# Kernel optimization log

Hardware: AMD Instinct MI355X
Metric: run time of the kernel (lower is better)

## Reference

```python
import jax, jax.numpy as jnp
import numpy as np

N_NODES = 100000
N_EDGES = 1200000
D_IN = 64
D_HID = 64
BN_EPS = 1e-5


def setup_inputs() -> dict:
    key = jax.random.key(0)
    ks = jax.random.split(key, 16)
    x = jax.random.normal(ks[0], (N_NODES, D_IN), dtype=jnp.float32)
    edge_index = jax.random.randint(ks[1], (2, N_EDGES), 0, N_NODES, dtype=jnp.int64)
    s = 1.0 / np.sqrt(D_HID)
    W1 = jax.random.uniform(ks[2], (D_IN, D_HID), jnp.float32, -s, s)
    b1 = jax.random.uniform(ks[3], (D_HID,), jnp.float32, -s, s)
    W2 = jax.random.uniform(ks[4], (D_HID, D_HID), jnp.float32, -s, s)
    b2 = jax.random.uniform(ks[5], (D_HID,), jnp.float32, -s, s)
    W3 = jax.random.uniform(ks[6], (D_HID, D_HID), jnp.float32, -s, s)
    b3 = jax.random.uniform(ks[7], (D_HID,), jnp.float32, -s, s)
    gamma1 = jnp.ones((D_HID,), jnp.float32)
    beta1 = jnp.zeros((D_HID,), jnp.float32)
    gamma2 = jnp.ones((D_HID,), jnp.float32)
    beta2 = jnp.zeros((D_HID,), jnp.float32)
    return {"x": x, "edge_index": edge_index, "batch_size": 1,
            "W1": W1, "b1": b1, "gamma1": gamma1, "beta1": beta1,
            "W2": W2, "b2": b2, "gamma2": gamma2, "beta2": beta2,
            "W3": W3, "b3": b3}


def _gcn_norm(edge_index, n):
    # PyG GCNConv: add self-loops, symmetric normalization D^-1/2 (A+I) D^-1/2
    loop = jnp.arange(n, dtype=edge_index.dtype)
    src = jnp.concatenate([edge_index[0], loop])
    dst = jnp.concatenate([edge_index[1], loop])
    deg = jax.ops.segment_sum(jnp.ones_like(dst, dtype=jnp.float32), dst, num_segments=n)
    dinv = jnp.where(deg > 0, jax.lax.rsqrt(jnp.maximum(deg, 1.0)), 0.0)
    norm = dinv[src] * dinv[dst]  # [E + N]
    return src, dst, norm


def _gcn_conv(h, W, b, src, dst, norm, n):
    h = h @ W                      # [N, D]
    msg = h[src] * norm[:, None]   # gather + scale, [E+N, D]
    out = jax.ops.segment_sum(msg, dst, num_segments=n)  # scatter-add
    return out + b


def _bn_train(h, gamma, beta):
    # BatchNorm1d over nodes, training-mode (biased batch statistics)
    m = h.mean(axis=0)
    v = h.var(axis=0)
    return (h - m) * jax.lax.rsqrt(v + BN_EPS) * gamma + beta


def reference(x, edge_index, batch_size,
              W1, b1, gamma1, beta1, W2, b2, gamma2, beta2, W3, b3):
    n = x.shape[0]
    src, dst, norm = _gcn_norm(edge_index, n)
    h = _gcn_conv(x, W1, b1, src, dst, norm, n)
    h = jax.nn.relu(_bn_train(h, gamma1, beta1))
    h = _gcn_conv(h, W2, b2, src, dst, norm, n)
    h = jax.nn.relu(_bn_train(h, gamma2, beta2))
    h = _gcn_conv(h, W3, b3, src, dst, norm, n)
    return h  # output_type == 'hidden'
```

## Files before the change

kernel.cpp:

```cpp
#include <hip/hip_runtime.h>
#include <hip/hip_bf16.h>

#define D 64

typedef __attribute__((ext_vector_type(8))) short bf16x8;
typedef __attribute__((ext_vector_type(8))) unsigned short u16x8;
typedef __attribute__((ext_vector_type(4))) float f32x4;

__device__ __forceinline__ short f2bf(float x) {
    unsigned u = __float_as_uint(x);
    unsigned r = (u + 0x7fffu + ((u >> 16) & 1u)) >> 16;
    return (short)r;
}
__device__ __forceinline__ float bf2f(unsigned short u) {
    return __uint_as_float((unsigned)u << 16);
}

__global__ void detect_kernel(const unsigned int* e32, int* flag) {
    __shared__ int nz;
    if (threadIdx.x == 0) nz = 0;
    __syncthreads();
    if (e32[2 * threadIdx.x + 1] != 0) nz = 1;
    __syncthreads();
    if (threadIdx.x == 0) *flag = (nz == 0) ? 1 : 0;
}

__device__ __forceinline__ int load_idx(const void* e, int is64, long long i) {
    if (is64) return (int)((const long long*)e)[i];
    return ((const int*)e)[i];
}

#define NBLK 256

__global__ __launch_bounds__(256) void bucket_count_kernel(
    const void* edges, const int* flag, int* pbh, int E, int shift) {
    __shared__ int h[512];
    for (int i = threadIdx.x; i < 512; i += 256) h[i] = 0;
    __syncthreads();
    int is64 = *flag;
    int chunk = (E + gridDim.x - 1) / gridDim.x;
    int s0 = blockIdx.x * chunk;
    int s1 = min(E, s0 + chunk);
    for (int e = s0 + (int)threadIdx.x; e < s1; e += 256) {
        int d = load_idx(edges, is64, (long long)E + e);
        atomicAdd(&h[d >> shift], 1);
    }
    __syncthreads();
    for (int i = threadIdx.x; i < 512; i += 256) pbh[blockIdx.x * 512 + i] = h[i];
}

__global__ __launch_bounds__(256) void colscan_kernel(int* pbh, int* btot) {
    int b = blockIdx.x;
    int k = threadIdx.x;
    __shared__ int sA[256], sB[256];
    int v = pbh[k * 512 + b];
    sA[k] = v;
    __syncthreads();
    int* src = sA;
    int* dst = sB;
    for (int d = 1; d < 256; d <<= 1) {
        dst[k] = src[k] + (k >= d ? src[k - d] : 0);
        __syncthreads();
        int* t = src; src = dst; dst = t;
    }
    pbh[k * 512 + b] = src[k] - v;
    if (k == 255) btot[b] = src[255];
}

__global__ __launch_bounds__(512) void basescan_kernel(const int* btot, int* bbase, int E) {
    __shared__ int sA[512], sB[512];
    int b = threadIdx.x;
    int v = btot[b];
    sA[b] = v;
    __syncthreads();
    int* src = sA;
    int* dst = sB;
    for (int d = 1; d < 512; d <<= 1) {
        dst[b] = src[b] + (b >= d ? src[b - d] : 0);
        __syncthreads();
        int* t = src; src = dst; dst = t;
    }
    bbase[b] = src[b] - v;
    if (b == 0) bbase[512] = E;
}

__global__ __launch_bounds__(256) void bucket_scatter_kernel(
    const void* edges, const int* flag, const int* pbh, const int* bbase,
    unsigned* staging, int E, int shift) {
    __shared__ int cur[512];
    for (int i = threadIdx.x; i < 512; i += 256)
        cur[i] = pbh[blockIdx.x * 512 + i] + bbase[i];
    __syncthreads();
    int is64 = *flag;
    int chunk = (E + gridDim.x - 1) / gridDim.x;
    int s0 = blockIdx.x * chunk;
    int s1 = min(E, s0 + chunk);
    unsigned mask = (unsigned)((1 << shift) - 1);
    for (int e = s0 + (int)threadIdx.x; e < s1; e += 256) {
        int s = load_idx(edges, is64, e);
        int d = load_idx(edges, is64, (long long)E + e);
        int b = d >> shift;
        int pos = atomicAdd(&cur[b], 1);
        staging[pos] = ((unsigned)s << shift) | ((unsigned)d & mask);
    }
}

__global__ __launch_bounds__(256) void bucket_fill_kernel(
    const unsigned* __restrict__ staging, const int* __restrict__ bbase,
    int* __restrict__ offs, float* __restrict__ dinv, int* __restrict__ srcs,
    int shift, int n, int E) {
    int b = blockIdx.x;
    int bstart = bbase[b], bend = bbase[b + 1];
    int bsz = 1 << shift;
    unsigned mask = (unsigned)(bsz - 1);
    int v0 = b << shift;
    int nloc = min(bsz, n - v0);

    __shared__ int cnt[512], cur[512], sA[512], sB[512];
    for (int i = threadIdx.x; i < bsz; i += 256) cnt[i] = 0;
    __syncthreads();
    for (int idx = bstart + (int)threadIdx.x; idx < bend; idx += 256)
        atomicAdd(&cnt[staging[idx] & mask], 1);
    __syncthreads();
    for (int i = threadIdx.x; i < bsz; i += 256) sA[i] = cnt[i];
    __syncthreads();
    int* src = sA;
    int* dst = sB;
    for (int d = 1; d < bsz; d <<= 1) {
        for (int i = threadIdx.x; i < bsz; i += 256)
            dst[i] = src[i] + (i >= d ? src[i - d] : 0);
        __syncthreads();
        int* t = src; src = dst; dst = t;
    }
    for (int i = threadIdx.x; i < bsz; i += 256) {
        int excl = src[i] - cnt[i];
        cur[i] = excl;
        if (i < nloc) {
            offs[v0 + i] = bstart + excl;
            dinv[v0 + i] = rsqrtf((float)(cnt[i] + 1));
        }
    }
    if (b == 0 && threadIdx.x == 0) offs[n] = E;
    __syncthreads();
    for (int idx = bstart + (int)threadIdx.x; idx < bend; idx += 256) {
        unsigned u = staging[idx];
        int ld = (int)(u & mask);
        int pos = atomicAdd(&cur[ld], 1);
        srcs[bstart + pos] = (int)(u >> shift);
    }
}

#define DBIN 256

__global__ __launch_bounds__(256) void deg_count_kernel(
    const int* __restrict__ offs, int* __restrict__ pdh, int n) {
    __shared__ int h[DBIN];
    for (int i = threadIdx.x; i < DBIN; i += 256) h[i] = 0;
    __syncthreads();
    int chunk = (n + gridDim.x - 1) / gridDim.x;
    int s0 = blockIdx.x * chunk;
    int s1 = min(n, s0 + chunk);
    for (int v = s0 + (int)threadIdx.x; v < s1; v += 256) {
        int d = min(offs[v + 1] - offs[v], DBIN - 1);
        atomicAdd(&h[d], 1);
    }
    __syncthreads();
    for (int i = threadIdx.x; i < DBIN; i += 256) pdh[blockIdx.x * DBIN + i] = h[i];
}

__global__ __launch_bounds__(256) void deg_colscan_kernel(int* pdh, int* dtot) {
    int b = blockIdx.x;
    int k = threadIdx.x;
    __shared__ int sA[256], sB[256];
    int v = pdh[k * DBIN + b];
    sA[k] = v;
    __syncthreads();
    int* src = sA;
    int* dst = sB;
    for (int d = 1; d < 256; d <<= 1) {
        dst[k] = src[k] + (k >= d ? src[k - d] : 0);
        __syncthreads();
        int* t = src; src = dst; dst = t;
    }
    pdh[k * DBIN + b] = src[k] - v;
    if (k == 255) dtot[b] = src[255];
}

__global__ __launch_bounds__(256) void deg_base_kernel(const int* dtot, int* dbase) {
    __shared__ int sA[256], sB[256];
    int b = threadIdx.x;
    int v = dtot[b];
    sA[b] = v;
    __syncthreads();
    int* src = sA;
    int* dst = sB;
    for (int d = 1; d < 256; d <<= 1) {
        dst[b] = src[b] + (b >= d ? src[b - d] : 0);
        __syncthreads();
        int* t = src; src = dst; dst = t;
    }
    dbase[b] = src[b] - v;
}

__global__ __launch_bounds__(256) void deg_scatter_kernel(
    const int* __restrict__ offs, const int* __restrict__ pdh, const int* __restrict__ dbase,
    int* __restrict__ perm, int* __restrict__ pj0, int* __restrict__ plen, int n) {
    __shared__ int cur[DBIN];
    for (int i = threadIdx.x; i < DBIN; i += 256)
        cur[i] = pdh[blockIdx.x * DBIN + i] + dbase[i];
    __syncthreads();
    int chunk = (n + gridDim.x - 1) / gridDim.x;
    int s0 = blockIdx.x * chunk;
    int s1 = min(n, s0 + chunk);
    for (int v = s0 + (int)threadIdx.x; v < s1; v += 256) {
        int a = offs[v];
        int d = offs[v + 1] - a;
        int bin = min(d, DBIN - 1);
        int pos = atomicAdd(&cur[bin], 1);
        perm[pos] = v;
        pj0[pos] = a;
        plen[pos] = d;
    }
}

__global__ __launch_bounds__(256) void mm_bn_kernel(
    const float* __restrict__ Xf, const unsigned short* __restrict__ Xb, int x_is_bf16,
    const float* __restrict__ W,
    const float* __restrict__ stats, const float* __restrict__ gamma,
    const float* __restrict__ beta, int use_bn, float inv_n,
    const float* __restrict__ dinv,
    unsigned short* __restrict__ Y, int n) {
    int lane = threadIdx.x & 63;
    int m = lane & 15;
    int quad = lane >> 4;

    float sc[16], sh[16];
#pragma unroll
    for (int s = 0; s < 2; s++) {
#pragma unroll
        for (int j = 0; j < 8; j++) {
            float scale = 1.f, shift = 0.f;
            if (use_bn) {
                int f = s * 32 + quad * 8 + j;
                float mean = stats[f] * inv_n;
                float var = stats[64 + f] * inv_n - mean * mean;
                float rs = rsqrtf(var + 1e-5f);
                scale = rs * gamma[f];
                shift = beta[f] - mean * scale;
            }
            sc[s * 8 + j] = scale;
            sh[s * 8 + j] = shift;
        }
    }

    bf16x8 bfrag[4][2];
#pragma unroll
    for (int nt = 0; nt < 4; nt++) {
#pragma unroll
        for (int s = 0; s < 2; s++) {
#pragma unroll
            for (int j = 0; j < 8; j++) {
                int k = s * 32 + quad * 8 + j;
                bfrag[nt][s][j] = f2bf(W[k * 64 + nt * 16 + m]);
            }
        }
    }

    int wave = blockIdx.x * 4 + (threadIdx.x >> 6);
    int nwaves = gridDim.x * 4;
    int ntiles = (n + 15) >> 4;
    const f32x4 zero = {0.f, 0.f, 0.f, 0.f};

    for (int t = wave; t < ntiles; t += nwaves) {
        int r = t * 16 + m;
        if (r >= n) r = n - 1;
        float av[16];
        if (x_is_bf16) {
            const unsigned short* xr = Xb + (long long)r * 64;
            u16x8 u0 = *(const u16x8*)(xr + quad * 8);
            u16x8 u1 = *(const u16x8*)(xr + 32 + quad * 8);
#pragma unroll
            for (int j = 0; j < 8; j++) {
                av[j] = bf2f(u0[j]);
                av[8 + j] = bf2f(u1[j]);
            }
        } else {
            const float* xr = Xf + (long long)r * 64;
            f32x4 a0 = *(const f32x4*)(xr + quad * 8);
            f32x4 a1 = *(const f32x4*)(xr + quad * 8 + 4);
            f32x4 a2 = *(const f32x4*)(xr + 32 + quad * 8);
            f32x4 a3 = *(const f32x4*)(xr + 32 + quad * 8 + 4);
#pragma unroll
            for (int j = 0; j < 4; j++) {
                av[j] = a0[j];
                av[4 + j] = a1[j];
                av[8 + j] = a2[j];
                av[12 + j] = a3[j];
            }
        }
        bf16x8 A0, A1;
#pragma unroll
        for (int j = 0; j < 8; j++) {
            float v0 = av[j] * sc[j] + sh[j];
            float v1 = av[8 + j] * sc[8 + j] + sh[8 + j];
            if (use_bn) {
                v0 = fmaxf(v0, 0.f);
                v1 = fmaxf(v1, 0.f);
            }
            A0[j] = f2bf(v0);
            A1[j] = f2bf(v1);
        }

        f32x4 acc[4];
#pragma unroll
        for (int nt = 0; nt < 4; nt++) {
            acc[nt] = __builtin_amdgcn_mfma_f32_16x16x32_bf16(A0, bfrag[nt][0], zero, 0, 0, 0);
            acc[nt] = __builtin_amdgcn_mfma_f32_16x16x32_bf16(A1, bfrag[nt][1], acc[nt], 0, 0, 0);
        }

        int row0 = t * 16 + quad * 4;
        float dv[4];
#pragma unroll
        for (int i = 0; i < 4; i++) {
            int rr = row0 + i;
            dv[i] = (rr < n) ? dinv[rr] : 0.f;
        }
#pragma unroll
        for (int nt = 0; nt < 4; nt++) {
#pragma unroll
            for (int i = 0; i < 4; i++) {
                int rr = row0 + i;
                if (rr < n)
                    Y[(long long)rr * 64 + nt * 16 + m] = (unsigned short)f2bf(acc[nt][i] * dv[i]);
            }
        }
    }
}

__global__ __launch_bounds__(256) void agg_kernel(
    const unsigned short* __restrict__ T,
    const int* __restrict__ perm,
    const int* __restrict__ pj0,
    const int* __restrict__ plen,
    const int* __restrict__ srcs,
    const float* __restrict__ dinv,
    const float* __restrict__ bias,
    unsigned short* __restrict__ out16,
    float* __restrict__ out32, int out_bf16,
    float* __restrict__ stats, int do_stats,
    int n) {
    __shared__ float S[128];
    if (do_stats) {
        if (threadIdx.x < 128) S[threadIdx.x] = 0.f;
        __syncthreads();
    }
    int lane = threadIdx.x & 63;
    int sub = lane >> 3;
    int c = lane & 7;
    int wave = blockIdx.x * 4 + (threadIdx.x >> 6);
    int nwaves = gridDim.x * 4;
    int ngrp = (n + 7) >> 3;
    f32x4 bi0 = *(const f32x4*)(bias + c * 8);
    f32x4 bi1 = *(const f32x4*)(bias + c * 8 + 4);
    float ss[8], sq[8];
#pragma unroll
    for (int i = 0; i < 8; i++) { ss[i] = 0.f; sq[i] = 0.f; }

    const char* Tb = (const char*)T;
    unsigned coff = (unsigned)c << 4;

    for (int g = wave; g < ngrp; g += nwaves) {
        int i = g * 8 + sub;
        int valid = i < n;
        int ic = valid ? i : n - 1;
        int v = perm[ic];
        int j0 = pj0[ic];
        int len = plen[ic];
        u16x8 sv = *(const u16x8*)(Tb + (((unsigned)v << 7) + coff));
        float acc[8];
#pragma unroll
        for (int q = 0; q < 8; q++) acc[q] = bf2f(sv[q]);

        int j = j0, j1 = j0 + len;
        for (; j + 8 <= j1; j += 8) {
            int sid[8];
#pragma unroll
            for (int u = 0; u < 8; u++) sid[u] = srcs[j + u];
            u16x8 r[8];
#pragma unroll
            for (int u = 0; u < 8; u++)
                r[u] = *(const u16x8*)(Tb + (((unsigned)sid[u] << 7) + coff));
#pragma unroll
            for (int u = 0; u < 8; u++) {
#pragma unroll
                for (int q = 0; q < 8; q++) acc[q] += bf2f(r[u][q]);
            }
        }
        if (j < j1) {
            int sid[8];
            float w[8];
#pragma unroll
            for (int u = 0; u < 8; u++) {
                int jj = j + u;
                int live = jj < j1;
                int jc = live ? jj : j1 - 1;
                int s = srcs[jc];
                sid[u] = live ? s : v;
                w[u] = live ? 1.f : 0.f;
            }
            u16x8 r[8];
#pragma unroll
            for (int u = 0; u < 8; u++)
                r[u] = *(const u16x8*)(Tb + (((unsigned)sid[u] << 7) + coff));
#pragma unroll
            for (int u = 0; u < 8; u++) {
#pragma unroll
                for (int q = 0; q < 8; q++) acc[q] += w[u] * bf2f(r[u][q]);
            }
        }

        float dv = dinv[v];
        float val[8];
#pragma unroll
        for (int q = 0; q < 4; q++) {
            val[q] = dv * acc[q] + bi0[q];
            val[4 + q] = dv * acc[4 + q] + bi1[q];
        }
        if (valid) {
            if (out_bf16) {
                u16x8 o;
#pragma unroll
                for (int q = 0; q < 8; q++) o[q] = (unsigned short)f2bf(val[q]);
                *(u16x8*)((char*)out16 + (((unsigned)v << 7) + coff)) = o;
            } else {
                f32x4 o0 = {val[0], val[1], val[2], val[3]};
                f32x4 o1 = {val[4], val[5], val[6], val[7]};
                float* op = out32 + (((unsigned)v << 6) + ((unsigned)c << 3));
                *(f32x4*)op = o0;
                *(f32x4*)(op + 4) = o1;
            }
            if (do_stats) {
#pragma unroll
                for (int q = 0; q < 8; q++) {
                    ss[q] += val[q];
                    sq[q] += val[q] * val[q];
                }
            }
        }
    }
    if (do_stats) {
#pragma unroll
        for (int q = 0; q < 8; q++) {
            atomicAdd(&S[c * 8 + q], ss[q]);
            atomicAdd(&S[64 + c * 8 + q], sq[q]);
        }
        __syncthreads();
        if (threadIdx.x < 128) atomicAdd(&stats[threadIdx.x], S[threadIdx.x]);
    }
}

extern "C" void kernel_launch(void* const* d_in, const int* in_sizes, int n_in,
                              void* d_out, int out_size, void* d_ws, size_t ws_size,
                              hipStream_t stream) {
    const float* x = (const float*)d_in[0];
    const void* edges = d_in[1];
    const float* W1 = (const float*)d_in[3];
    const float* b1 = (const float*)d_in[4];
    const float* gamma1 = (const float*)d_in[5];
    const float* beta1 = (const float*)d_in[6];
    const float* W2 = (const float*)d_in[7];
    const float* b2 = (const float*)d_in[8];
    const float* gamma2 = (const float*)d_in[9];
    const float* beta2 = (const float*)d_in[10];
    const float* W3 = (const float*)d_in[11];
    const float* b3 = (const float*)d_in[12];

    const int N = in_sizes[0] / D;
    const int E = in_sizes[1] / 2;
    const float inv_n = 1.f / (float)N;

    int shift = 8;
    while ((((long long)N - 1) >> shift) + 1 > 512) shift++;
    const int nbuk = (int)(((long long)N - 1) >> shift) + 1;

    char* ws = (char*)d_ws;
    size_t off = 0;
    auto alloc = [&](size_t bytes) -> void* {
        void* p = ws + off;
        off = (off + bytes + 255) & ~(size_t)255;
        return p;
    };
    float*    dinv    = (float*)   alloc((size_t)N * 4);
    int*      offs    = (int*)     alloc((size_t)(N + 1) * 4);
    int*      srcs    = (int*)     alloc((size_t)E * 4);
    unsigned* staging = (unsigned*)alloc((size_t)E * 4);
    int*      pbh     = (int*)     alloc((size_t)NBLK * 512 * 4);
    int*      btot    = (int*)     alloc(512 * 4);
    int*      bbase   = (int*)     alloc(513 * 4);
    int*      flag    = (int*)     alloc(4);
    float*    stats   = (float*)   alloc(256 * 4);
    int*      pdh     = (int*)     alloc((size_t)NBLK * DBIN * 4);
    int*      dtot    = (int*)     alloc(DBIN * 4);
    int*      dbase   = (int*)     alloc(DBIN * 4);
    int*      perm    = (int*)     alloc((size_t)N * 4);
    int*      pj0v    = (int*)     alloc((size_t)N * 4);
    int*      plenv   = (int*)     alloc((size_t)N * 4);
    unsigned short* bufA = (unsigned short*)alloc((size_t)N * D * 2);
    unsigned short* hbuf = (unsigned short*)alloc((size_t)N * D * 2);
    float*    outf    = (float*)d_out;

    const int AGGB = 1563;
    const int MMB  = 782;

    detect_kernel<<<1, 256, 0, stream>>>((const unsigned int*)edges, flag);
    bucket_count_kernel<<<NBLK, 256, 0, stream>>>(edges, flag, pbh, E, shift);
    colscan_kernel<<<512, 256, 0, stream>>>(pbh, btot);
    basescan_kernel<<<1, 512, 0, stream>>>(btot, bbase, E);
    bucket_scatter_kernel<<<NBLK, 256, 0, stream>>>(edges, flag, pbh, bbase, staging, E, shift);
    bucket_fill_kernel<<<nbuk, 256, 0, stream>>>(staging, bbase, offs, dinv, srcs, shift, N, E);
    deg_count_kernel<<<NBLK, 256, 0, stream>>>(offs, pdh, N);
    deg_colscan_kernel<<<DBIN, 256, 0, stream>>>(pdh, dtot);
    deg_base_kernel<<<1, 256, 0, stream>>>(dtot, dbase);
    deg_scatter_kernel<<<NBLK, 256, 0, stream>>>(offs, pdh, dbase, perm, pj0v, plenv, N);
    hipMemsetAsync(stats, 0, 256 * 4, stream);

    mm_bn_kernel<<<MMB, 256, 0, stream>>>(x, nullptr, 0, W1, nullptr, nullptr, nullptr, 0,
                                          inv_n, dinv, bufA, N);
    agg_kernel<<<AGGB, 256, 0, stream>>>(bufA, perm, pj0v, plenv, srcs, dinv, b1,
                                         hbuf, nullptr, 1, stats, 1, N);

    mm_bn_kernel<<<MMB, 256, 0, stream>>>(nullptr, hbuf, 1, W2, stats, gamma1, beta1, 1,
                                          inv_n, dinv, bufA, N);
    agg_kernel<<<AGGB, 256, 0, stream>>>(bufA, perm, pj0v, plenv, srcs, dinv, b2,
                                         hbuf, nullptr, 1, stats + 128, 1, N);

    mm_bn_kernel<<<MMB, 256, 0, stream>>>(nullptr, hbuf, 1, W3, stats + 128, gamma2, beta2, 1,
                                          inv_n, dinv, bufA, N);
    agg_kernel<<<AGGB, 256, 0, stream>>>(bufA, perm, pj0v, plenv, srcs, dinv, b3,
                                         nullptr, outf, 0, nullptr, 0, N);
}
```

Before: 364.4 us.

## Pad CSR neighbor lists to 16 with zero-row sentinel and pre-shifted indices

Each node's neighbor list is padded to a multiple of 16 entries. Padding slots point at an extra zero row appended to the feature buffer, and indices are stored pre-multiplied by the row stride. The aggregation loop becomes branch-free 16-wide blocks with vectorised int4 index loads, and the tail handling disappears. Nodes are grouped by block count in descending order, with dinv permuted alongside them. BN stats are now accumulated with per-row shared atomics instead of register partials, and the grid size is computed from N. The costs are extra padded gathers, more shared-memory atomic contention, and a larger index buffer.

```diff
diff --git a/kernel.cpp b/kernel.cpp
--- a/kernel.cpp
+++ b/kernel.cpp
@@ -31,6 +31,7 @@
 }
 
 #define NBLK 256
+#define PADB 4096
 
 __global__ __launch_bounds__(256) void bucket_count_kernel(
     const void* edges, const int* flag, int* pbh, int E, int shift) {
@@ -107,14 +108,16 @@
 
 __global__ __launch_bounds__(256) void bucket_fill_kernel(
     const unsigned* __restrict__ staging, const int* __restrict__ bbase,
-    int* __restrict__ offs, float* __restrict__ dinv, int* __restrict__ srcs,
-    int shift, int n, int E) {
+    int* __restrict__ pj0n, int* __restrict__ degv, float* __restrict__ dinv,
+    int* __restrict__ srcs2, int shift, int n, int E) {
     int b = blockIdx.x;
     int bstart = bbase[b], bend = bbase[b + 1];
     int bsz = 1 << shift;
     unsigned mask = (unsigned)(bsz - 1);
     int v0 = b << shift;
     int nloc = min(bsz, n - v0);
+    int Pb = ((bstart + 15) & ~15) + PADB * b;
+    int sentinel = n << 7;
 
     __shared__ int cnt[512], cur[512], sA[512], sB[512];
     for (int i = threadIdx.x; i < bsz; i += 256) cnt[i] = 0;
@@ -122,7 +125,7 @@
     for (int idx = bstart + (int)threadIdx.x; idx < bend; idx += 256)
         atomicAdd(&cnt[staging[idx] & mask], 1);
     __syncthreads();
-    for (int i = threadIdx.x; i < bsz; i += 256) sA[i] = cnt[i];
+    for (int i = threadIdx.x; i < bsz; i += 256) sA[i] = (cnt[i] + 15) & ~15;
     __syncthreads();
     int* src = sA;
     int* dst = sB;
@@ -133,37 +136,43 @@
         int* t = src; src = dst; dst = t;
     }
     for (int i = threadIdx.x; i < bsz; i += 256) {
-        int excl = src[i] - cnt[i];
-        cur[i] = excl;
+        int c = cnt[i];
+        int pc = (c + 15) & ~15;
+        int st = Pb + src[i] - pc;
+        cur[i] = st;
         if (i < nloc) {
-            offs[v0 + i] = bstart + excl;
-            dinv[v0 + i] = rsqrtf((float)(cnt[i] + 1));
-        }
-    }
-    if (b == 0 && threadIdx.x == 0) offs[n] = E;
+            pj0n[v0 + i] = st;
+            degv[v0 + i] = c;
+            dinv[v0 + i] = rsqrtf((float)(c + 1));
+            for (int s2 = c; s2 < pc; s2++) srcs2[st + s2] = sentinel;
+        }
+    }
     __syncthreads();
     for (int idx = bstart + (int)threadIdx.x; idx < bend; idx += 256) {
         unsigned u = staging[idx];
         int ld = (int)(u & mask);
         int pos = atomicAdd(&cur[ld], 1);
-        srcs[bstart + pos] = (int)(u >> shift);
+        srcs2[pos] = (int)(u >> shift) << 7;
     }
 }
 
 #define DBIN 256
 
+__device__ __forceinline__ int deg_bin(int deg) {
+    int nb = (deg + 15) >> 4;
+    return (DBIN - 1) - min(nb, DBIN - 1);
+}
+
 __global__ __launch_bounds__(256) void deg_count_kernel(
-    const int* __restrict__ offs, int* __restrict__ pdh, int n) {
+    const int* __restrict__ degv, int* __restrict__ pdh, int n) {
     __shared__ int h[DBIN];
     for (int i = threadIdx.x; i < DBIN; i += 256) h[i] = 0;
     __syncthreads();
     int chunk = (n + gridDim.x - 1) / gridDim.x;
     int s0 = blockIdx.x * chunk;
     int s1 = min(n, s0 + chunk);
-    for (int v = s0 + (int)threadIdx.x; v < s1; v += 256) {
-        int d = min(offs[v + 1] - offs[v], DBIN - 1);
-        atomicAdd(&h[d], 1);
-    }
+    for (int v = s0 + (int)threadIdx.x; v < s1; v += 256)
+        atomicAdd(&h[deg_bin(degv[v])], 1);
     __syncthreads();
     for (int i = threadIdx.x; i < DBIN; i += 256) pdh[blockIdx.x * DBIN + i] = h[i];
 }
@@ -203,8 +212,11 @@
 }
 
 __global__ __launch_bounds__(256) void deg_scatter_kernel(
-    const int* __restrict__ offs, const int* __restrict__ pdh, const int* __restrict__ dbase,
-    int* __restrict__ perm, int* __restrict__ pj0, int* __restrict__ plen, int n) {
+    const int* __restrict__ degv, const int* __restrict__ pj0n,
+    const float* __restrict__ dinv,
+    const int* __restrict__ pdh, const int* __restrict__ dbase,
+    int* __restrict__ perm, int* __restrict__ pj0, int* __restrict__ pnb,
+    float* __restrict__ pdinv, int n) {
     __shared__ int cur[DBIN];
     for (int i = threadIdx.x; i < DBIN; i += 256)
         cur[i] = pdh[blockIdx.x * DBIN + i] + dbase[i];
@@ -213,13 +225,12 @@
     int s0 = blockIdx.x * chunk;
     int s1 = min(n, s0 + chunk);
     for (int v = s0 + (int)threadIdx.x; v < s1; v += 256) {
-        int a = offs[v];
-        int d = offs[v + 1] - a;
-        int bin = min(d, DBIN - 1);
-        int pos = atomicAdd(&cur[bin], 1);
+        int d = degv[v];
+        int pos = atomicAdd(&cur[deg_bin(d)], 1);
         perm[pos] = v;
-        pj0[pos] = a;
-        plen[pos] = d;
+        pj0[pos] = pj0n[v];
+        pnb[pos] = (d + 15) >> 4;
+        pdinv[pos] = dinv[v];
     }
 }
 
@@ -341,9 +352,9 @@
     const unsigned short* __restrict__ T,
     const int* __restrict__ perm,
     const int* __restrict__ pj0,
-    const int* __restrict__ plen,
-    const int* __restrict__ srcs,
-    const float* __restrict__ dinv,
+    const int* __restrict__ pnb,
+    const float* __restrict__ pdinv,
+    const int* __restrict__ srcs2,
     const float* __restrict__ bias,
     unsigned short* __restrict__ out16,
     float* __restrict__ out32, int out_bf16,
@@ -362,9 +373,6 @@
     int ngrp = (n + 7) >> 3;
     f32x4 bi0 = *(const f32x4*)(bias + c * 8);
     f32x4 bi1 = *(const f32x4*)(bias + c * 8 + 4);
-    float ss[8], sq[8];
-#pragma unroll
-    for (int i = 0; i < 8; i++) { ss[i] = 0.f; sq[i] = 0.f; }
 
     const char* Tb = (const char*)T;
     unsigned coff = (unsigned)c << 4;
@@ -374,52 +382,45 @@
         int valid = i < n;
         int ic = valid ? i : n - 1;
         int v = perm[ic];
-        int j0 = pj0[ic];
-        int len = plen[ic];
+        int j = pj0[ic];
+        int nb = pnb[ic];
+        float dv = pdinv[ic];
         u16x8 sv = *(const u16x8*)(Tb + (((unsigned)v << 7) + coff));
         float acc[8];
 #pragma unroll
         for (int q = 0; q < 8; q++) acc[q] = bf2f(sv[q]);
 
-        int j = j0, j1 = j0 + len;
-        for (; j + 8 <= j1; j += 8) {
-            int sid[8];
-#pragma unroll
-            for (int u = 0; u < 8; u++) sid[u] = srcs[j + u];
-            u16x8 r[8];
-#pragma unroll
-            for (int u = 0; u < 8; u++)
-                r[u] = *(const u16x8*)(Tb + (((unsigned)sid[u] << 7) + coff));
-#pragma unroll
-            for (int u = 0; u < 8; u++) {
+        for (int bb = 0; bb < nb; bb++) {
+            const int* sp = srcs2 + j;
+            int4 s0 = *(const int4*)sp;
+            int4 s1 = *(const int4*)(sp + 4);
+            int4 s2 = *(const int4*)(sp + 8);
+            int4 s3 = *(const int4*)(sp + 12);
+            u16x8 r[16];
+            r[0]  = *(const u16x8*)(Tb + ((unsigned)s0.x + coff));
+            r[1]  = *(const u16x8*)(Tb + ((unsigned)s0.y + coff));
+            r[2]  = *(const u16x8*)(Tb + ((unsigned)s0.z + coff));
+            r[3]  = *(const u16x8*)(Tb + ((unsigned)s0.w + coff));
+            r[4]  = *(const u16x8*)(Tb + ((unsigned)s1.x + coff));
+            r[5]  = *(const u16x8*)(Tb + ((unsigned)s1.y + coff));
+            r[6]  = *(const u16x8*)(Tb + ((unsigned)s1.z + coff));
+            r[7]  = *(const u16x8*)(Tb + ((unsigned)s1.w + coff));
+            r[8]  = *(const u16x8*)(Tb + ((unsigned)s2.x + coff));
+            r[9]  = *(const u16x8*)(Tb + ((unsigned)s2.y + coff));
+            r[10] = *(const u16x8*)(Tb + ((unsigned)s2.z + coff));
+            r[11] = *(const u16x8*)(Tb + ((unsigned)s2.w + coff));
+            r[12] = *(const u16x8*)(Tb + ((unsigned)s3.x + coff));
+            r[13] = *(const u16x8*)(Tb + ((unsigned)s3.y + coff));
+            r[14] = *(const u16x8*)(Tb + ((unsigned)s3.z + coff));
+            r[15] = *(const u16x8*)(Tb + ((unsigned)s3.w + coff));
+#pragma unroll
+            for (int u = 0; u < 16; u++) {
 #pragma unroll
                 for (int q = 0; q < 8; q++) acc[q] += bf2f(r[u][q]);
             }
-        }
-        if (j < j1) {
-            int sid[8];
-            float w[8];
-#pragma unroll
-            for (int u = 0; u < 8; u++) {
-                int jj = j + u;
-                int live = jj < j1;
-                int jc = live ? jj : j1 - 1;
-                int s = srcs[jc];
-                sid[u] = live ? s : v;
-                w[u] = live ? 1.f : 0.f;
-            }
-            u16x8 r[8];
-#pragma unroll
-            for (int u = 0; u < 8; u++)
-                r[u] = *(const u16x8*)(Tb + (((unsigned)sid[u] << 7) + coff));
-#pragma unroll
-            for (int u = 0; u < 8; u++) {
-#pragma unroll
-                for (int q = 0; q < 8; q++) acc[q] += w[u] * bf2f(r[u][q]);
-            }
-        }
-
-        float dv = dinv[v];
+            j += 16;
+        }
+
         float val[8];
 #pragma unroll
         for (int q = 0; q < 4; q++) {
@@ -442,18 +443,13 @@
             if (do_stats) {
 #pragma unroll
                 for (int q = 0; q < 8; q++) {
-                    ss[q] += val[q];
-                    sq[q] += val[q] * val[q];
+                    atomicAdd(&S[c * 8 + q], val[q]);
+                    atomicAdd(&S[64 + c * 8 + q], val[q] * val[q]);
                 }
             }
         }
     }
     if (do_stats) {
-#pragma unroll
-        for (int q = 0; q < 8; q++) {
-            atomicAdd(&S[c * 8 + q], ss[q]);
-            atomicAdd(&S[64 + c * 8 + q], sq[q]);
-        }
         __syncthreads();
         if (threadIdx.x < 128) atomicAdd(&stats[threadIdx.x], S[threadIdx.x]);
     }
@@ -491,8 +487,9 @@
         return p;
     };
     float*    dinv    = (float*)   alloc((size_t)N * 4);
-    int*      offs    = (int*)     alloc((size_t)(N + 1) * 4);
-    int*      srcs    = (int*)     alloc((size_t)E * 4);
+    int*      pj0n    = (int*)     alloc((size_t)N * 4);
+    int*      degv    = (int*)     alloc((size_t)N * 4);
+    int*      srcs2   = (int*)     alloc(((size_t)E + (size_t)PADB * 512 + 64) * 4);
     unsigned* staging = (unsigned*)alloc((size_t)E * 4);
     int*      pbh     = (int*)     alloc((size_t)NBLK * 512 * 4);
     int*      btot    = (int*)     alloc(512 * 4);
@@ -504,12 +501,14 @@
     int*      dbase   = (int*)     alloc(DBIN * 4);
     int*      perm    = (int*)     alloc((size_t)N * 4);
     int*      pj0v    = (int*)     alloc((size_t)N * 4);
-    int*      plenv   = (int*)     alloc((size_t)N * 4);
-    unsigned short* bufA = (unsigned short*)alloc((size_t)N * D * 2);
+    int*      pnbv    = (int*)     alloc((size_t)N * 4);
+    float*    pdinv   = (float*)   alloc((size_t)N * 4);
+    unsigned short* bufA = (unsigned short*)alloc((size_t)(N + 1) * D * 2);
     unsigned short* hbuf = (unsigned short*)alloc((size_t)N * D * 2);
     float*    outf    = (float*)d_out;
 
-    const int AGGB = 1563;
+    const int ngrp = (N + 7) >> 3;
+    const int AGGB = (ngrp + 3) / 4;
     const int MMB  = 782;
 
     detect_kernel<<<1, 256, 0, stream>>>((const unsigned int*)edges, flag);
@@ -517,25 +516,28 @@
     colscan_kernel<<<512, 256, 0, stream>>>(pbh, btot);
     basescan_kernel<<<1, 512, 0, stream>>>(btot, bbase, E);
     bucket_scatter_kernel<<<NBLK, 256, 0, stream>>>(edges, flag, pbh, bbase, staging, E, shift);
-    bucket_fill_kernel<<<nbuk, 256, 0, stream>>>(staging, bbase, offs, dinv, srcs, shift, N, E);
-    deg_count_kernel<<<NBLK, 256, 0, stream>>>(offs, pdh, N);
+    bucket_fill_kernel<<<nbuk, 256, 0, stream>>>(staging, bbase, pj0n, degv, dinv, srcs2,
+                                                 shift, N, E);
+    deg_count_kernel<<<NBLK, 256, 0, stream>>>(degv, pdh, N);
     deg_colscan_kernel<<<DBIN, 256, 0, stream>>>(pdh, dtot);
     deg_base_kernel<<<1, 256, 0, stream>>>(dtot, dbase);
-    deg_scatter_kernel<<<NBLK, 256, 0, stream>>>(offs, pdh, dbase, perm, pj0v, plenv, N);
+    deg_scatter_kernel<<<NBLK, 256, 0, stream>>>(degv, pj0n, dinv, pdh, dbase,
+                                                 perm, pj0v, pnbv, pdinv, N);
     hipMemsetAsync(stats, 0, 256 * 4, stream);
+    hipMemsetAsync(bufA + (size_t)N * D, 0, D * 2, stream);
 
     mm_bn_kernel<<<MMB, 256, 0, stream>>>(x, nullptr, 0, W1, nullptr, nullptr, nullptr, 0,
                                           inv_n, dinv, bufA, N);
-    agg_kernel<<<AGGB, 256, 0, stream>>>(bufA, perm, pj0v, plenv, srcs, dinv, b1,
+    agg_kernel<<<AGGB, 256, 0, stream>>>(bufA, perm, pj0v, pnbv, pdinv, srcs2, b1,
                                          hbuf, nullptr, 1, stats, 1, N);
 
     mm_bn_kernel<<<MMB, 256, 0, stream>>>(nullptr, hbuf, 1, W2, stats, gamma1, beta1, 1,
                                           inv_n, dinv, bufA, N);
-    agg_kernel<<<AGGB, 256, 0, stream>>>(bufA, perm, pj0v, plenv, srcs, dinv, b2,
+    agg_kernel<<<AGGB, 256, 0, stream>>>(bufA, perm, pj0v, pnbv, pdinv, srcs2, b2,
                                          hbuf, nullptr, 1, stats + 128, 1, N);
 
     mm_bn_kernel<<<MMB, 256, 0, stream>>>(nullptr, hbuf, 1, W3, stats + 128, gamma2, beta2, 1,
                                           inv_n, dinv, bufA, N);
-    agg_kernel<<<AGGB, 256, 0, stream>>>(bufA, perm, pj0v, plenv, srcs, dinv, b3,
+    agg_kernel<<<AGGB, 256, 0, stream>>>(bufA, perm, pj0v, pnbv, pdinv, srcs2, b3,
                                          nullptr, outf, 0, nullptr, 0, N);
 }
```

Measured after the change: 446.9 us. +22.6%, slower.
